# Kernel optimization log

Measured on AMD Instinct MI355X. Metric: run time of the kernel, lower is better.

The kernel has to match this reference:

```python
import jax, jax.numpy as jnp
import numpy as np

N = 524288      # total trajectory tokens
D_MODEL = 256
HIDDEN = 512
OUT_DIM = 32
N_TYPES = 4


def setup_inputs() -> dict:
    key = jax.random.key(0)
    k1, k2, k3, k4 = jax.random.split(key, 4)
    x = jax.random.normal(k1, (N, D_MODEL), dtype=jnp.float32)
    types = jax.random.randint(k2, (N,), 0, N_TYPES, dtype=jnp.int64)
    W1 = jax.random.normal(k3, (N_TYPES, D_MODEL, HIDDEN), dtype=jnp.float32) / np.sqrt(D_MODEL)
    b1 = jnp.zeros((N_TYPES, HIDDEN), dtype=jnp.float32)
    W2 = jax.random.normal(k4, (N_TYPES, HIDDEN, OUT_DIM), dtype=jnp.float32) / np.sqrt(HIDDEN)
    b2 = jnp.zeros((N_TYPES, OUT_DIM), dtype=jnp.float32)
    return {"x": x, "types": types, "W1": W1, "b1": b1, "W2": W2, "b2": b2}


def reference(x, types, W1, b1, W2, b2):
    # Type-masked gather -> per-type MLP decode -> scatter back to original order.
    # The gather/argsort-scatter of the torch code is equivalent (for equal
    # per-type output dims) to computing each type's decoder and selecting the
    # rows where types == type_id; we loop over the small fixed set of types.
    n_types = W1.shape[0]
    out = jnp.zeros((x.shape[0], W2.shape[-1]), dtype=x.dtype)
    for t in range(n_types):
        h = jax.nn.relu(x @ W1[t] + b1[t])          # [N, HIDDEN]
        y = h @ W2[t] + b2[t]                        # [N, OUT_DIM]
        out = jnp.where((types == t)[:, None], y, out)
    return out
```

## Files before the change

kernel.cpp:

```cpp
#include <hip/hip_runtime.h>
#include <hip/hip_bf16.h>
#include <hip/hip_fp16.h>

#define N_TOK 524288
#define DM 256
#define HID 512
#define OUTD 32
#define NTYPE 4
#define BM 128
#define HC 32
#define NCHUNK (HID / HC)
#define CHUNK_BYTES (HC * DM * 2)
#define NBLK 512
#define GX 1152
#define HS_STRIDE 80

typedef _Float16 half8 __attribute__((ext_vector_type(8)));
typedef float f32x4 __attribute__((ext_vector_type(4)));


__global__ void count_kernel(const int* __restrict__ types, int* __restrict__ bc) {
    __shared__ int c[NTYPE];
    int tid = threadIdx.x;
    if (tid < NTYPE) c[tid] = 0;
    __syncthreads();
    int b = blockIdx.x;
    int lane = tid & 63;
    #pragma unroll
    for (int j = 0; j < 4; ++j) {
        int t = types[b * 1024 + j * 256 + tid];
        #pragma unroll
        for (int tt = 0; tt < NTYPE; ++tt) {
            unsigned long long mask = __ballot(t == tt);
            if (lane == 0) atomicAdd(&c[tt], __popcll(mask));
        }
    }
    __syncthreads();
    if (tid < NTYPE) bc[tid * NBLK + b] = c[tid];
}

__global__ void scan_blocks_kernel(const int* __restrict__ bc,
                                   int* __restrict__ bb,
                                   int* __restrict__ meta) {
    __shared__ int totals[NTYPE];
    __shared__ int typeoff[NTYPE];
    int wave = threadIdx.x >> 6, lane = threadIdx.x & 63;
    int excl[NBLK / 64];
    int running = 0;
    #pragma unroll
    for (int it = 0; it < NBLK / 64; ++it) {
        int v = bc[wave * NBLK + it * 64 + lane];
        int s = v;
        #pragma unroll
        for (int d = 1; d < 64; d <<= 1) {
            int u = __shfl_up(s, d);
            if (lane >= d) s += u;
        }
        excl[it] = running + s - v;
        running += __shfl(s, 63);
    }
    if (lane == 0) totals[wave] = running;
    __syncthreads();
    if (threadIdx.x == 0) {
        int off = 0;
        for (int tt = 0; tt < NTYPE; ++tt) {
            typeoff[tt] = off;
            meta[tt] = totals[tt];
            meta[4 + tt] = off;
            off += totals[tt];
        }
    }
    __syncthreads();
    #pragma unroll
    for (int it = 0; it < NBLK / 64; ++it)
        bb[wave * NBLK + it * 64 + lane] = typeoff[wave] + excl[it];
}

__global__ void scatter2_kernel(const int* __restrict__ types,
                                const int* __restrict__ bb,
                                int* __restrict__ idx) {
    __shared__ int base[NTYPE];
    __shared__ int wcnt[4][NTYPE];
    int b = blockIdx.x;
    int tid = threadIdx.x, wave = tid >> 6, lane = tid & 63;
    if (tid < NTYPE) base[tid] = bb[tid * NBLK + b];
    #pragma unroll
    for (int j = 0; j < 4; ++j) {
        __syncthreads();
        int i = b * 1024 + j * 256 + tid;
        int t = types[i];
        int rank = 0;
        #pragma unroll
        for (int tt = 0; tt < NTYPE; ++tt) {
            unsigned long long mask = __ballot(t == tt);
            if (t == tt) rank = __popcll(mask & ((1ull << lane) - 1ull));
            if (lane == 0) wcnt[wave][tt] = __popcll(mask);
        }
        __syncthreads();
        int pre = 0;
        for (int w = 0; w < wave; ++w) pre += wcnt[w][t];
        idx[base[t] + pre + rank] = i;
        __syncthreads();
        if (tid < NTYPE) {
            int tot = 0;
            #pragma unroll
            for (int w = 0; w < 4; ++w) tot += wcnt[w][tid];
            base[tid] += tot;
        }
    }
}


__global__ void wprep_kernel(const float* __restrict__ W1, const float* __restrict__ W2,
                             _Float16* __restrict__ W1T, _Float16* __restrict__ W2T) {
    int i = blockIdx.x * blockDim.x + threadIdx.x;
    if (i < NTYPE * HID * DM) {
        int t = i / (HID * DM);
        int r = i - t * (HID * DM);
        int byteoff = r * 2;
        int hc = byteoff / CHUNK_BYTES;
        int rem = byteoff - hc * CHUNK_BYTES;
        int hr = rem >> 9;
        int brow = rem & 511;
        int d = (brow ^ ((hr & 7) << 4)) >> 1;
        int h = hc * HC + hr;
        W1T[i] = (_Float16)W1[(t * DM + d) * HID + h];
    }
    if (i < NTYPE * OUTD * HID) {
        int t = i / (OUTD * HID);
        int r = i - t * (OUTD * HID);
        int o = r / HID;
        int h = r - o * HID;
        W2T[i] = (_Float16)W2[(t * HID + h) * OUTD + o];
    }
}


__launch_bounds__(256)
__global__ void fused_mlp_kernel(const float* __restrict__ x,
                                 const int* __restrict__ meta,
                                 const int* __restrict__ idx,
                                 const _Float16* __restrict__ W1T,
                                 const _Float16* __restrict__ W2T,
                                 const float* __restrict__ b1,
                                 const float* __restrict__ b2,
                                 float* __restrict__ out) {
    const int t = blockIdx.y;
    const int cnt = meta[t];
    const int row_base = blockIdx.x * BM;
    if (row_base >= cnt) return;
    const int* idx_t = idx + meta[4 + t];

    __shared__ __align__(16) char W1sB[2][CHUNK_BYTES];
    __shared__ __align__(16) char HsB[4][32 * HS_STRIDE];
    __shared__ float b1s[HID];

    const int tid = threadIdx.x;
    const int wave = tid >> 6;
    const int lane = tid & 63;
    const int l15 = lane & 15;
    const int lg = lane >> 4;

    {
        float2 bv = *(const float2*)(b1 + t * HID + tid * 2);
        b1s[tid * 2] = bv.x;
        b1s[tid * 2 + 1] = bv.y;
    }

    half8 afrag[2][8];
    #pragma unroll
    for (int mt = 0; mt < 2; ++mt) {
        int rl = wave * 32 + mt * 16 + l15;
        int rglob = idx_t[min(row_base + rl, cnt - 1)];
        const float* xr = x + (size_t)rglob * DM;
        #pragma unroll
        for (int kk = 0; kk < 8; ++kk) {
            int k0 = kk * 32 + lg * 8;
            f32x4 v0 = __builtin_nontemporal_load((const f32x4*)(xr + k0));
            f32x4 v1 = __builtin_nontemporal_load((const f32x4*)(xr + k0 + 4));
            half8 h;
            h[0] = (_Float16)v0[0]; h[1] = (_Float16)v0[1];
            h[2] = (_Float16)v0[2]; h[3] = (_Float16)v0[3];
            h[4] = (_Float16)v1[0]; h[5] = (_Float16)v1[1];
            h[6] = (_Float16)v1[2]; h[7] = (_Float16)v1[3];
            afrag[mt][kk] = h;
        }
    }

    const f32x4 fzero = {0.f, 0.f, 0.f, 0.f};
    f32x4 acc2[2][2];
    #pragma unroll
    for (int mt = 0; mt < 2; ++mt)
        #pragma unroll
        for (int nt = 0; nt < 2; ++nt)
            acc2[mt][nt] = fzero;

    const char* w1base = (const char*)(W1T + (size_t)t * HID * DM);
    const _Float16* w2t_t = W2T + (size_t)t * OUTD * HID;
    char* myHs = HsB[wave];

    #pragma unroll
    for (int it = 0; it < 4; ++it) {
        __builtin_amdgcn_global_load_lds(
            (const __attribute__((address_space(1))) void*)(w1base + it * 4096 + tid * 16),
            (__attribute__((address_space(3))) void*)(&W1sB[0][it * 4096 + tid * 16]),
            16, 0, 0);
    }
    half8 w2A[2], w2B[2];
    #pragma unroll
    for (int nt = 0; nt < 2; ++nt)
        w2A[nt] = *(const half8*)(w2t_t + (nt * 16 + l15) * HID + lg * 8);
    __syncthreads();

#define CHUNK_BODY(HCI, W2USE, W2FILL)                                          \
    {                                                                           \
        const int hc = (HCI);                                                   \
        const char* cur = W1sB[hc & 1];                                         \
        if (hc + 1 < NCHUNK) {                                                  \
            const char* src = w1base + (size_t)(hc + 1) * CHUNK_BYTES;          \
            char* dst = W1sB[(hc + 1) & 1];                                     \
            _Pragma("unroll")                                                   \
            for (int it = 0; it < 4; ++it) {                                    \
                __builtin_amdgcn_global_load_lds(                               \
                    (const __attribute__((address_space(1))) void*)(src + it * 4096 + tid * 16), \
                    (__attribute__((address_space(3))) void*)(dst + it * 4096 + tid * 16),       \
                    16, 0, 0);                                                  \
            }                                                                   \
        }                                                                       \
        {                 \
            int hn = (hc + 1) & 15;                                             \
            _Pragma("unroll")                                                   \
            for (int nt = 0; nt < 2; ++nt)                                      \
                W2FILL[nt] = *(const half8*)(w2t_t + (nt * 16 + l15) * HID + hn * HC + lg * 8); \
        }                                                                       \
        f32x4 acc1[2][2];                                                       \
        _Pragma("unroll")                                                       \
        for (int mt = 0; mt < 2; ++mt)                                          \
            _Pragma("unroll")                                                   \
            for (int nt = 0; nt < 2; ++nt)                                      \
                acc1[mt][nt] = fzero;                                           \
        _Pragma("unroll")                                                       \
        for (int kk = 0; kk < 8; ++kk) {                                        \
            half8 bfr[2];                                                       \
            _Pragma("unroll")                                                   \
            for (int nt = 0; nt < 2; ++nt) {                                    \
                int hr = nt * 16 + l15;                                         \
                bfr[nt] = *(const half8*)(cur + hr * 512 +                      \
                            ((kk * 64 + lg * 16) ^ ((hr & 7) << 4)));           \
            }                                                                   \
            _Pragma("unroll")                                                   \
            for (int mt = 0; mt < 2; ++mt)                                      \
                _Pragma("unroll")                                               \
                for (int nt = 0; nt < 2; ++nt)                                  \
                    acc1[mt][nt] = __builtin_amdgcn_mfma_f32_16x16x32_f16(      \
                        afrag[mt][kk], bfr[nt], acc1[mt][nt], 0, 0, 0);         \
        }                                                                       \
             \
        _Pragma("unroll")                                                       \
        for (int nt = 0; nt < 2; ++nt) {                                        \
            int col = nt * 16 + l15;                                            \
            float bias = b1s[hc * HC + col];                                    \
            _Pragma("unroll")                                                   \
            for (int mt = 0; mt < 2; ++mt) {                                    \
                _Pragma("unroll")                                               \
                for (int j = 0; j < 4; ++j) {                                   \
                    float v = fmaxf(acc1[mt][nt][j] + bias, 0.f);               \
                    int rl = mt * 16 + lg * 4 + j;                              \
                    *(_Float16*)(myHs + rl * HS_STRIDE + col * 2) = (_Float16)v;\
                }                                                               \
            }                                                                   \
        }                                                                       \
                                          \
        half8 a2[2];                                                            \
        _Pragma("unroll")                                                       \
        for (int mt = 0; mt < 2; ++mt) {                                        \
            int rl = mt * 16 + l15;                                             \
            a2[mt] = *(const half8*)(myHs + rl * HS_STRIDE + lg * 16);          \
        }                                                                       \
        _Pragma("unroll")                                                       \
        for (int mt = 0; mt < 2; ++mt)                                          \
            _Pragma("unroll")                                                   \
            for (int nt = 0; nt < 2; ++nt)                                      \
                acc2[mt][nt] = __builtin_amdgcn_mfma_f32_16x16x32_f16(          \
                    a2[mt], W2USE[nt], acc2[mt][nt], 0, 0, 0);                  \
        __syncthreads();   \
    }

    #pragma unroll
    for (int h2 = 0; h2 < NCHUNK; h2 += 2) {
        CHUNK_BODY(h2, w2A, w2B);
        CHUNK_BODY(h2 + 1, w2B, w2A);
    }
#undef CHUNK_BODY

    const int m = min(BM, cnt - row_base);
    #pragma unroll
    for (int mt = 0; mt < 2; ++mt) {
        #pragma unroll
        for (int j = 0; j < 4; ++j) {
            int rloc = wave * 32 + mt * 16 + lg * 4 + j;
            if (rloc < m) {
                int gr = idx_t[row_base + rloc];
                #pragma unroll
                for (int nt = 0; nt < 2; ++nt) {
                    int col = nt * 16 + l15;
                    float v = acc2[mt][nt][j] + b2[t * OUTD + col];
                    __builtin_nontemporal_store(v, &out[(size_t)gr * OUTD + col]);
                }
            }
        }
    }
}


extern "C" void kernel_launch(void* const* d_in, const int* in_sizes, int n_in,
                              void* d_out, int out_size, void* d_ws, size_t ws_size,
                              hipStream_t stream) {
    const float* x   = (const float*)d_in[0];
    const int* types = (const int*)d_in[1];
    const float* W1  = (const float*)d_in[2];
    const float* b1  = (const float*)d_in[3];
    const float* W2  = (const float*)d_in[4];
    const float* b2  = (const float*)d_in[5];
    float* out = (float*)d_out;

    char* ws = (char*)d_ws;
    int* meta = (int*)ws;
    int* idx = (int*)(ws + 64);
    _Float16* W1T = (_Float16*)(ws + 64 + 4 * (size_t)N_TOK);
    _Float16* W2T = W1T + (size_t)NTYPE * HID * DM;
    int* bc = (int*)W1T;
    int* bb = bc + NTYPE * NBLK;

    count_kernel<<<NBLK, 256, 0, stream>>>(types, bc);
    scan_blocks_kernel<<<1, 256, 0, stream>>>(bc, bb, meta);
    scatter2_kernel<<<NBLK, 256, 0, stream>>>(types, bb, idx);
    wprep_kernel<<<(NTYPE * HID * DM) / 256, 256, 0, stream>>>(W1, W2, W1T, W2T);

    dim3 grid(GX, NTYPE);
    fused_mlp_kernel<<<grid, 256, 0, stream>>>(x, meta, idx, W1T, W2T, b1, b2, out);
}
```

Before: 272.5 us.

## Double rows per block and compact grid into 1D per-type tile list

Raises the row tile from 128 to 256 rows per block, with each wave handling four 16-row MFMA tiles, so every W1/W2 chunk staged in LDS is reused across twice as many tokens. The 2D grid, which launched many blocks that exit at once, is replaced by a 1D grid whose per-type tile offsets are computed in the scan kernel. Launch bounds now ask for two blocks per CU. The cost is much higher register pressure from doubled A fragments and accumulators, a risk of spills, and fewer blocks in total.

```diff
diff --git a/kernel.cpp b/kernel.cpp
--- a/kernel.cpp
+++ b/kernel.cpp
@@ -7,12 +7,13 @@
 #define HID 512
 #define OUTD 32
 #define NTYPE 4
-#define BM 128
+#define BM 256
+#define MT 4
 #define HC 32
 #define NCHUNK (HID / HC)
 #define CHUNK_BYTES (HC * DM * 2)
 #define NBLK 512
-#define GX 1152
+#define GX1D (N_TOK / BM + NTYPE)
 #define HS_STRIDE 80
 
 typedef _Float16 half8 __attribute__((ext_vector_type(8)));
@@ -62,13 +63,16 @@
     if (lane == 0) totals[wave] = running;
     __syncthreads();
     if (threadIdx.x == 0) {
-        int off = 0;
+        int off = 0, toff = 0;
         for (int tt = 0; tt < NTYPE; ++tt) {
             typeoff[tt] = off;
             meta[tt] = totals[tt];
             meta[4 + tt] = off;
+            meta[8 + tt] = toff;
             off += totals[tt];
-        }
+            toff += (totals[tt] + BM - 1) / BM;
+        }
+        meta[12] = toff;
     }
     __syncthreads();
     #pragma unroll
@@ -136,7 +140,7 @@
 }
 
 
-__launch_bounds__(256)
+__launch_bounds__(256, 2)
 __global__ void fused_mlp_kernel(const float* __restrict__ x,
                                  const int* __restrict__ meta,
                                  const int* __restrict__ idx,
@@ -145,14 +149,15 @@
                                  const float* __restrict__ b1,
                                  const float* __restrict__ b2,
                                  float* __restrict__ out) {
-    const int t = blockIdx.y;
+    const int b = blockIdx.x;
+    if (b >= meta[12]) return;
+    const int t = (b >= meta[9]) + (b >= meta[10]) + (b >= meta[11]);
     const int cnt = meta[t];
-    const int row_base = blockIdx.x * BM;
-    if (row_base >= cnt) return;
+    const int row_base = (b - meta[8 + t]) * BM;
     const int* idx_t = idx + meta[4 + t];
 
     __shared__ __align__(16) char W1sB[2][CHUNK_BYTES];
-    __shared__ __align__(16) char HsB[4][32 * HS_STRIDE];
+    __shared__ __align__(16) char HsB[4][64 * HS_STRIDE];
     __shared__ float b1s[HID];
 
     const int tid = threadIdx.x;
@@ -167,10 +172,10 @@
         b1s[tid * 2 + 1] = bv.y;
     }
 
-    half8 afrag[2][8];
-    #pragma unroll
-    for (int mt = 0; mt < 2; ++mt) {
-        int rl = wave * 32 + mt * 16 + l15;
+    half8 afrag[MT][8];
+    #pragma unroll
+    for (int mt = 0; mt < MT; ++mt) {
+        int rl = wave * 64 + mt * 16 + l15;
         int rglob = idx_t[min(row_base + rl, cnt - 1)];
         const float* xr = x + (size_t)rglob * DM;
         #pragma unroll
@@ -188,9 +193,9 @@
     }
 
     const f32x4 fzero = {0.f, 0.f, 0.f, 0.f};
-    f32x4 acc2[2][2];
-    #pragma unroll
-    for (int mt = 0; mt < 2; ++mt)
+    f32x4 acc2[MT][2];
+    #pragma unroll
+    for (int mt = 0; mt < MT; ++mt)
         #pragma unroll
         for (int nt = 0; nt < 2; ++nt)
             acc2[mt][nt] = fzero;
@@ -233,9 +238,9 @@
             for (int nt = 0; nt < 2; ++nt)                                      \
                 W2FILL[nt] = *(const half8*)(w2t_t + (nt * 16 + l15) * HID + hn * HC + lg * 8); \
         }                                                                       \
-        f32x4 acc1[2][2];                                                       \
-        _Pragma("unroll")                                                       \
-        for (int mt = 0; mt < 2; ++mt)                                          \
+        f32x4 acc1[MT][2];                                                      \
+        _Pragma("unroll")                                                       \
+        for (int mt = 0; mt < MT; ++mt)                                         \
             _Pragma("unroll")                                                   \
             for (int nt = 0; nt < 2; ++nt)                                      \
                 acc1[mt][nt] = fzero;                                           \
@@ -249,19 +254,19 @@
                             ((kk * 64 + lg * 16) ^ ((hr & 7) << 4)));           \
             }                                                                   \
             _Pragma("unroll")                                                   \
-            for (int mt = 0; mt < 2; ++mt)                                      \
+            for (int mt = 0; mt < MT; ++mt)                                     \
                 _Pragma("unroll")                                               \
                 for (int nt = 0; nt < 2; ++nt)                                  \
                     acc1[mt][nt] = __builtin_amdgcn_mfma_f32_16x16x32_f16(      \
                         afrag[mt][kk], bfr[nt], acc1[mt][nt], 0, 0, 0);         \
         }                                                                       \
-             \
+            \
         _Pragma("unroll")                                                       \
         for (int nt = 0; nt < 2; ++nt) {                                        \
             int col = nt * 16 + l15;                                            \
             float bias = b1s[hc * HC + col];                                    \
             _Pragma("unroll")                                                   \
-            for (int mt = 0; mt < 2; ++mt) {                                    \
+            for (int mt = 0; mt < MT; ++mt) {                                   \
                 _Pragma("unroll")                                               \
                 for (int j = 0; j < 4; ++j) {                                   \
                     float v = fmaxf(acc1[mt][nt][j] + bias, 0.f);               \
@@ -271,14 +276,14 @@
             }                                                                   \
         }                                                                       \
                                           \
-        half8 a2[2];                                                            \
-        _Pragma("unroll")                                                       \
-        for (int mt = 0; mt < 2; ++mt) {                                        \
+        half8 a2[MT];                                                           \
+        _Pragma("unroll")                                                       \
+        for (int mt = 0; mt < MT; ++mt) {                                       \
             int rl = mt * 16 + l15;                                             \
             a2[mt] = *(const half8*)(myHs + rl * HS_STRIDE + lg * 16);          \
         }                                                                       \
         _Pragma("unroll")                                                       \
-        for (int mt = 0; mt < 2; ++mt)                                          \
+        for (int mt = 0; mt < MT; ++mt)                                         \
             _Pragma("unroll")                                                   \
             for (int nt = 0; nt < 2; ++nt)                                      \
                 acc2[mt][nt] = __builtin_amdgcn_mfma_f32_16x16x32_f16(          \
@@ -295,10 +300,10 @@
 
     const int m = min(BM, cnt - row_base);
     #pragma unroll
-    for (int mt = 0; mt < 2; ++mt) {
+    for (int mt = 0; mt < MT; ++mt) {
         #pragma unroll
         for (int j = 0; j < 4; ++j) {
-            int rloc = wave * 32 + mt * 16 + lg * 4 + j;
+            int rloc = wave * 64 + mt * 16 + lg * 4 + j;
             if (rloc < m) {
                 int gr = idx_t[row_base + rloc];
                 #pragma unroll
@@ -337,6 +342,5 @@
     scatter2_kernel<<<NBLK, 256, 0, stream>>>(types, bb, idx);
     wprep_kernel<<<(NTYPE * HID * DM) / 256, 256, 0, stream>>>(W1, W2, W1T, W2T);
 
-    dim3 grid(GX, NTYPE);
-    fused_mlp_kernel<<<grid, 256, 0, stream>>>(x, meta, idx, W1T, W2T, b1, b2, out);
-}
+    fused_mlp_kernel<<<GX1D, 256, 0, stream>>>(x, meta, idx, W1T, W2T, b1, b2, out);
+}
```

New measurement: 280.1 us. 2.8% more time.
